# Kernel optimization log

Measured on AMD Instinct MI355X. Metric: run time of the kernel, lower is better.

Reference implementation:

```python
import jax, jax.numpy as jnp
import numpy as np


def setup_inputs() -> dict:
    key = jax.random.key(0)
    X = jax.random.normal(key, (8, 4096, 1024), dtype=jnp.float32)
    return {"X": X}


def _pos_encoding(T, d, dtype):
    # P[pos, 2i]   = sin(pos / 10000^(2i/d))
    # P[pos, 2i+1] = cos(pos / 10000^(2i/d))
    pos = jnp.arange(T, dtype=dtype)[:, None]              # (T, 1)
    i = jnp.arange(d // 2, dtype=dtype)[None, :]           # (1, d/2)
    angle = pos / jnp.power(jnp.asarray(10000.0, dtype), (2.0 * i) / d)  # (T, d/2)
    pe = jnp.stack([jnp.sin(angle), jnp.cos(angle)], axis=-1)  # (T, d/2, 2)
    return pe.reshape(T, d)                                # interleaved sin/cos


def reference(X):
    B, T, d = X.shape
    pe = _pos_encoding(T, d, X.dtype)
    return X + pe[None, :, :]
```

## Files before the change

### kernel.cpp

```cpp
#include <hip/hip_runtime.h>
#include <math.h>


typedef float floatx4 __attribute__((ext_vector_type(4)));

__global__ __launch_bounds__(256) void pe_add_kernel(
    const float* __restrict__ X, float* __restrict__ out) {
    constexpr int B = 8, T = 4096, D = 1024;
    constexpr int D4 = D / 4;
    constexpr long long TD = (long long)T * D;

    const int idx = blockIdx.x * blockDim.x + threadIdx.x;
    const int t  = idx >> 8;
    const int c4 = idx & (D4 - 1);
    const int d0 = c4 * 4;

    const float L2_10000 = 13.287712379549449f;
    const float pos = (float)t;
    const float i0 = (float)(d0 >> 1);
    const float i1 = i0 + 1.0f;
    const float f0 = exp2f(-(2.0f * i0 / (float)D) * L2_10000);
    const float f1 = exp2f(-(2.0f * i1 / (float)D) * L2_10000);

    float s0, c0, s1, c1;
    sincosf(pos * f0, &s0, &c0);
    sincosf(pos * f1, &s1, &c1);

    floatx4 pe;
    pe.x = s0; pe.y = c0; pe.z = s1; pe.w = c1;
    const long long base = (long long)t * D + d0;

    #pragma unroll
    for (int b = 0; b < B; ++b) {
        const long long off = (long long)b * TD + base;
        floatx4 x = *reinterpret_cast<const floatx4*>(X + off);
        x += pe;
        __builtin_nontemporal_store(x, reinterpret_cast<floatx4*>(out + off));
    }
}

extern "C" void kernel_launch(void* const* d_in, const int* in_sizes, int n_in,
                              void* d_out, int out_size, void* d_ws, size_t ws_size,
                              hipStream_t stream) {
    const float* X = (const float*)d_in[0];
    float* out = (float*)d_out;
    constexpr int T = 4096, D = 1024;
    constexpr int threads = 256;
    constexpr int total = T * D / 4;
    constexpr int blocks = (total + threads - 1) / threads;
    pe_add_kernel<<<blocks, threads, 0, stream>>>(X, out);
}
```

Before: 47.93 us.

## Split batch across four thread groups, two batches per thread, regular stores

Each thread now handles two batch slices (b and b+4) rather than all eight, so four times as many threads are launched. The aim is more memory-level parallelism and occupancy to better saturate HBM bandwidth. The cost is that sin/cos positional-encoding values are recomputed four times as often. Nontemporal stores are also replaced with ordinary stores, which may change cache behaviour on writes.

```diff
diff --git a/kernel.cpp b/kernel.cpp
--- a/kernel.cpp
+++ b/kernel.cpp
@@ -6,14 +6,17 @@
 
 __global__ __launch_bounds__(256) void pe_add_kernel(
     const float* __restrict__ X, float* __restrict__ out) {
-    constexpr int B = 8, T = 4096, D = 1024;
+    constexpr int D = 1024;
     constexpr int D4 = D / 4;
-    constexpr long long TD = (long long)T * D;
+    constexpr int TD4 = 4096 * D4;
+    constexpr long long TD = (long long)4096 * D;
 
-    const int idx = blockIdx.x * blockDim.x + threadIdx.x;
-    const int t  = idx >> 8;
-    const int c4 = idx & (D4 - 1);
-    const int d0 = c4 * 4;
+    const int tid = blockIdx.x * blockDim.x + threadIdx.x;
+    const int bp  = tid >> 20;
+    const int rem = tid & (TD4 - 1);
+    const int t   = rem >> 8;
+    const int c4  = rem & (D4 - 1);
+    const int d0  = c4 * 4;
 
     const float L2_10000 = 13.287712379549449f;
     const float pos = (float)t;
@@ -28,15 +31,17 @@
 
     floatx4 pe;
     pe.x = s0; pe.y = c0; pe.z = s1; pe.w = c1;
+
     const long long base = (long long)t * D + d0;
+    const long long offA = (long long)bp * TD + base;
+    const long long offB = (long long)(bp + 4) * TD + base;
 
-    #pragma unroll
-    for (int b = 0; b < B; ++b) {
-        const long long off = (long long)b * TD + base;
-        floatx4 x = *reinterpret_cast<const floatx4*>(X + off);
-        x += pe;
-        __builtin_nontemporal_store(x, reinterpret_cast<floatx4*>(out + off));
-    }
+    floatx4 xa = *reinterpret_cast<const floatx4*>(X + offA);
+    floatx4 xb = *reinterpret_cast<const floatx4*>(X + offB);
+    xa += pe;
+    xb += pe;
+    *reinterpret_cast<floatx4*>(out + offA) = xa;
+    *reinterpret_cast<floatx4*>(out + offB) = xb;
 }
 
 extern "C" void kernel_launch(void* const* d_in, const int* in_sizes, int n_in,
@@ -44,9 +49,8 @@
                               hipStream_t stream) {
     const float* X = (const float*)d_in[0];
     float* out = (float*)d_out;
-    constexpr int T = 4096, D = 1024;
     constexpr int threads = 256;
-    constexpr int total = T * D / 4;
-    constexpr int blocks = (total + threads - 1) / threads;
+    constexpr int total = 4 * 4096 * 256;
+    constexpr int blocks = total / threads;
     pe_add_kernel<<<blocks, threads, 0, stream>>>(X, out);
 }
```

Result: faster. 43.14 us (-10.0%).
